# Kernel tuning notes

Hardware: AMD Instinct MI355X
Metric: run time of the kernel (lower is better)

The kernel has to match this reference:

```python
import math
import jax, jax.numpy as jnp
import numpy as np

D_MODEL = 512
H = 8          # head_num
HD = 64        # head_dim
ETA = 4
R = 8
D_FFC = 2048
EPS = 1e-6
GRU_BIAS = 2.0
T, B = 128, 32
TOTAL_PROJ = H * HD * 5 + H * ETA * 3  # 2656


def _layer_norm(x, g, b):
    m = x.mean(-1, keepdims=True)
    v = ((x - m) ** 2).mean(-1, keepdims=True)
    return (x - m) / jnp.sqrt(v + 1e-5) * g + b


def _outer(a, b):
    # a: (T,B,H,D), b: (T,B,H,E) -> (T,B,H,D*E), row-major over (D,E) like torch bmm+reshape
    t, bb, h, d = a.shape
    return (a[..., :, None] * b[..., None, :]).reshape(t, bb, h, d * b.shape[-1])


def _gru_gate(x, y, w, u):
    # GTrXL-style gating: x = residual stream, y = new signal. w,u: (3, d, d)
    r = jax.nn.sigmoid(y @ w[0].T + x @ u[0].T)
    z = jax.nn.sigmoid(y @ w[1].T + x @ u[1].T - GRU_BIAS)
    h = jnp.tanh(y @ w[2].T + (r * x) @ u[2].T)
    return (1.0 - z) * x + z * h


def _discounted_sum(prev, x, d):
    # y_t = d_t * y_{t-1} + x_t, y_{-1} = prev. x: (T, ...), d broadcastable to x.
    def step(c, xd):
        xi, di = xd
        nc = di * c + xi
        return nc, nc
    _, ys = jax.lax.scan(step, prev, (x, d))
    return ys


def setup_inputs() -> dict:
    key = jax.random.key(0)
    ks = jax.random.split(key, 12)
    sc_p = 1.0 / math.sqrt(D_MODEL)
    return {
        "inputs": jax.random.normal(ks[0], (T, B, D_MODEL), jnp.float32),
        "terminations": jax.random.randint(ks[1], (T, B), 0, 2).astype(jnp.int32),
        "tilde_k": jnp.zeros((B, R, H, ETA * HD), jnp.float32),
        "tilde_v": jnp.zeros((B, R, H, HD), jnp.float32),
        "s_prev": jnp.zeros((B, H, ETA * HD), jnp.float32),
        "tick": jnp.zeros((B, 1), jnp.float32),
        "w_proj": jax.random.normal(ks[2], (TOTAL_PROJ, D_MODEL), jnp.float32) * sc_p,
        "b_proj": jnp.zeros((TOTAL_PROJ,), jnp.float32),
        "w_attn": jax.random.normal(ks[3], (D_MODEL, H * HD), jnp.float32) * (1.0 / math.sqrt(H * HD)),
        "b_attn": jnp.zeros((D_MODEL,), jnp.float32),
        "ln1_g": jnp.ones((D_MODEL,), jnp.float32),
        "ln1_b": jnp.zeros((D_MODEL,), jnp.float32),
        "ln2_g": jnp.ones((D_MODEL,), jnp.float32),
        "ln2_b": jnp.zeros((D_MODEL,), jnp.float32),
        "gru1_w": jax.random.normal(ks[4], (3, D_MODEL, D_MODEL), jnp.float32) * sc_p,
        "gru1_u": jax.random.normal(ks[5], (3, D_MODEL, D_MODEL), jnp.float32) * sc_p,
        "gru2_w": jax.random.normal(ks[6], (3, D_MODEL, D_MODEL), jnp.float32) * sc_p,
        "gru2_u": jax.random.normal(ks[7], (3, D_MODEL, D_MODEL), jnp.float32) * sc_p,
        "ffc_w1": jax.random.normal(ks[8], (D_FFC, D_MODEL), jnp.float32) * sc_p,
        "ffc_b1": jnp.zeros((D_FFC,), jnp.float32),
        "ffc_w2": jax.random.normal(ks[9], (D_MODEL, D_FFC), jnp.float32) * (1.0 / math.sqrt(D_FFC)),
        "ffc_b2": jnp.zeros((D_MODEL,), jnp.float32),
    }


def _forward(inputs, terminations, tilde_k, tilde_v, s_prev, tick,
             w_proj, b_proj, w_attn, b_attn, ln1_g, ln1_b, ln2_g, ln2_b,
             gru1_w, gru1_u, gru2_w, gru2_u, ffc_w1, ffc_b1, ffc_w2, ffc_b2):
    t, bsz, _ = inputs.shape
    omegas = jnp.linspace(-math.pi, math.pi, R).astype(inputs.dtype)

    x_normed = _layer_norm(inputs, ln1_g, ln1_b)
    all_proj = x_normed @ w_proj.T + b_proj  # (T,B,2656)
    kqv_dim = H * HD * 5
    kqvbg = all_proj[..., :kqv_dim].reshape(t, bsz, H, 5, HD)
    p123 = all_proj[..., kqv_dim:].reshape(t, bsz, H, 3, ETA)

    keys = kqvbg[..., 0, :]
    queries = kqvbg[..., 1, :]
    values = kqvbg[..., 2, :]
    beta = jax.nn.sigmoid(kqvbg[..., 3, :])
    gammas = kqvbg[..., 4, :]
    p1, p2, p3 = p123[..., 0, :], p123[..., 1, :], p123[..., 2, :]

    keys_exp = _outer(jax.nn.relu(keys), jax.nn.relu(p1))          # (T,B,H,HD*ETA)
    queries_exp = _outer(jax.nn.relu(queries), jax.nn.relu(p2))
    gammas_exp = _outer(jax.nn.sigmoid(gammas), jax.nn.sigmoid(p3))

    ticks = tick[None] + jnp.arange(1, t + 1, dtype=tick.dtype).reshape(t, 1, 1)  # (T,B,1)
    occil = jnp.cos(ticks * omegas)  # (T,B,R)

    values_gated = values * beta                 # (T,B,H,HD)
    keys_gated = keys_exp * gammas_exp           # (T,B,H,HD*ETA)
    s_in = keys_gated
    values_osc = values_gated[:, :, None] * occil[..., None, None]  # (T,B,R,H,HD)
    keys_osc = keys_gated[:, :, None] * occil[..., None, None]      # (T,B,R,H,HD*ETA)

    term_mask = (1.0 - terminations.astype(inputs.dtype))[:, :, None, None]  # (T,B,1,1)
    discount_gamma = (1.0 - gammas_exp) * term_mask   # (T,B,H,HD*ETA)
    discount_beta = (1.0 - beta) * term_mask          # (T,B,H,HD)

    final_keys = _discounted_sum(tilde_k, keys_osc, discount_gamma[:, :, None])
    final_values = _discounted_sum(tilde_v, values_osc, discount_beta[:, :, None])
    final_s = _discounted_sum(s_prev, s_in, discount_gamma)

    kdq = (final_keys * queries_exp[:, :, None]).sum(-1)   # (T,B,R,H)
    kv = (final_values * kdq[..., None]).sum(2)             # (T,B,H,HD)
    norm = (final_s * queries_exp).sum(-1) + EPS            # (T,B,H)
    attn = kv / (2 * R * norm[..., None])
    attn = attn.reshape(t, bsz, H * HD) @ w_attn.T + b_attn  # (T,B,d_model)

    gating1 = _gru_gate(inputs, jax.nn.relu(attn), gru1_w, gru1_u)
    ffc_in = _layer_norm(gating1, ln2_g, ln2_b)
    ffc_out = jax.nn.relu(jax.nn.relu(ffc_in @ ffc_w1.T + ffc_b1) @ ffc_w2.T + ffc_b2)
    output = _gru_gate(gating1, ffc_out, gru2_w, gru2_u)
    return output


def reference(inputs, terminations, tilde_k, tilde_v, s_prev, tick,
              w_proj, b_proj, w_attn, b_attn, ln1_g, ln1_b, ln2_g, ln2_b,
              gru1_w, gru1_u, gru2_w, gru2_u, ffc_w1, ffc_b1, ffc_w2, ffc_b2):
    return _forward(inputs, terminations, tilde_k, tilde_v, s_prev, tick,
                    w_proj, b_proj, w_attn, b_attn, ln1_g, ln1_b, ln2_g, ln2_b,
                    gru1_w, gru1_u, gru2_w, gru2_u, ffc_w1, ffc_b1, ffc_w2, ffc_b2)
```

## Files before the change

kernel.cpp:

```cpp
#include <hip/hip_runtime.h>
#include <hip/hip_bf16.h>
#include <math.h>

#define DM   512
#define HH   8
#define RR   8
#define TT   128
#define BBATCH 32
#define MM   (TT*BBATCH)
#define NPROJ 2656
#define KQV  2560

typedef __attribute__((ext_vector_type(8))) short bf16x8;
typedef __attribute__((ext_vector_type(4))) float f32x4;

__device__ __forceinline__ float sigmoidf_(float x) {
    return 1.0f / (1.0f + __expf(-x));
}

__device__ __forceinline__ void gload_lds16(const void* g, void* l) {
    __builtin_amdgcn_global_load_lds(
        (const __attribute__((address_space(1))) unsigned int*)g,
        (__attribute__((address_space(3))) unsigned int*)l, 16, 0, 0);
}

template<int CTRL, int RMASK>
__device__ __forceinline__ float dpp_add_(float x) {
    union { float f; int i; } a, b;
    a.f = x;
    b.i = __builtin_amdgcn_update_dpp(0, a.i, CTRL, RMASK, 0xf, true);
    return x + b.f;
}
__device__ __forceinline__ float wave_sum_u(float x) {
    x = dpp_add_<0x111, 0xf>(x);
    x = dpp_add_<0x112, 0xf>(x);
    x = dpp_add_<0x114, 0xf>(x);
    x = dpp_add_<0x118, 0xf>(x);
    x = dpp_add_<0x142, 0xa>(x);
    x = dpp_add_<0x143, 0xc>(x);
    union { float f; int i; } s, t;
    s.f = x;
    t.i = __builtin_amdgcn_readlane(s.i, 63);
    return t.f;
}

struct F2B9 {
    const float* s[9];
    __hip_bfloat16* d[9];
    int cum[10];
};

__global__ __launch_bounds__(256) void f2b_ln_all(F2B9 a,
    const float* __restrict__ x, const float* __restrict__ g,
    const float* __restrict__ b, __hip_bfloat16* __restrict__ lnout)
{
    if (blockIdx.x < 8752) {
        int q = blockIdx.x * 256 + threadIdx.x;
        if (q >= a.cum[9]) return;
        int s = 0;
        #pragma unroll
        for (int i = 1; i < 9; ++i) s += (q >= a.cum[i]);
        int i4 = (q - a.cum[s]) * 4;
        float4 v = *(const float4*)(a.s[s] + i4);
        __hip_bfloat16* dst = a.d[s] + i4;
        dst[0] = __float2bfloat16(v.x);
        dst[1] = __float2bfloat16(v.y);
        dst[2] = __float2bfloat16(v.z);
        dst[3] = __float2bfloat16(v.w);
        return;
    }
    int row = blockIdx.x - 8752;
    int tid = threadIdx.x;
    const float* xr = x + (size_t)row * DM;
    float2 v = ((const float2*)xr)[tid];
    float s = v.x + v.y;
    #pragma unroll
    for (int off = 32; off; off >>= 1) s += __shfl_down(s, off);
    __shared__ float red[8];
    int wid = tid >> 6, lane = tid & 63;
    if (lane == 0) red[wid] = s;
    __syncthreads();
    if (tid == 0) red[0] = (red[0] + red[1] + red[2] + red[3]) * (1.0f / DM);
    __syncthreads();
    float mean = red[0];
    float dx = v.x - mean, dy = v.y - mean;
    float sq = dx*dx + dy*dy;
    #pragma unroll
    for (int off = 32; off; off >>= 1) sq += __shfl_down(sq, off);
    if (lane == 0) red[4 + wid] = sq;
    __syncthreads();
    if (tid == 0) red[1] = rsqrtf((red[4]+red[5]+red[6]+red[7]) * (1.0f/DM) + 1e-5f);
    __syncthreads();
    float rstd = red[1];
    float2 gg = ((const float2*)g)[tid];
    float2 bb = ((const float2*)b)[tid];
    __hip_bfloat16* orow = lnout + (size_t)row * DM;
    orow[2*tid+0] = __float2bfloat16(dx * rstd * gg.x + bb.x);
    orow[2*tid+1] = __float2bfloat16(dy * rstd * gg.y + bb.y);
}

__device__ __forceinline__ void gemm_core128(
    const __hip_bfloat16* __restrict__ A, const __hip_bfloat16* __restrict__ W,
    const float* __restrict__ bias,
    float* __restrict__ Cf, __hip_bfloat16* __restrict__ Cb,
    int N, int K, int act, int m0, int n0,
    __hip_bfloat16* As, __hip_bfloat16* Bs)
{
    int tid = threadIdx.x;
    int wave = tid >> 6, lane = tid & 63;
    int wm = (wave >> 1) * 64, wn = (wave & 1) * 64;
    int fr = lane & 15, fq = lane >> 4;

    f32x4 acc[4][4];
    #pragma unroll
    for (int i = 0; i < 4; ++i)
        #pragma unroll
        for (int j = 0; j < 4; ++j)
            acc[i][j] = (f32x4){0.f, 0.f, 0.f, 0.f};

    int sm0 = wave*16 + fr;
    int sm1 = sm0 + 64;
    int wr0 = n0 + sm0; if (wr0 >= N) wr0 = N - 1;
    int wr1 = n0 + sm1; if (wr1 >= N) wr1 = N - 1;
    const __hip_bfloat16* Ag0 = A + (size_t)(m0 + sm0) * K + fq*8;
    const __hip_bfloat16* Ag1 = A + (size_t)(m0 + sm1) * K + fq*8;
    const __hip_bfloat16* Wg0 = W + (size_t)wr0 * K + fq*8;
    const __hip_bfloat16* Wg1 = W + (size_t)wr1 * K + fq*8;

    for (int k0 = 0; k0 < K; k0 += 32) {
        gload_lds16(Ag0 + k0, As + (size_t)wave*512);
        gload_lds16(Ag1 + k0, As + (size_t)(wave+4)*512);
        gload_lds16(Wg0 + k0, Bs + (size_t)wave*512);
        gload_lds16(Wg1 + k0, Bs + (size_t)(wave+4)*512);
        __syncthreads();
        bf16x8 af[4], bfr[4];
        #pragma unroll
        for (int i = 0; i < 4; ++i) {
            af[i]  = *(const bf16x8*)(As + (size_t)(wm/16 + i)*512 + lane*8);
            bfr[i] = *(const bf16x8*)(Bs + (size_t)(wn/16 + i)*512 + lane*8);
        }
        #pragma unroll
        for (int mi = 0; mi < 4; ++mi)
            #pragma unroll
            for (int ni = 0; ni < 4; ++ni)
                acc[mi][ni] = __builtin_amdgcn_mfma_f32_16x16x32_bf16(
                    af[mi], bfr[ni], acc[mi][ni], 0, 0, 0);
        __syncthreads();
    }

    #pragma unroll
    for (int ni = 0; ni < 4; ++ni) {
        int n = n0 + wn + ni*16 + fr;
        bool nok = n < N;
        float bv = (bias && nok) ? bias[n] : 0.f;
        #pragma unroll
        for (int mi = 0; mi < 4; ++mi) {
            #pragma unroll
            for (int r = 0; r < 4; ++r) {
                int m = m0 + wm + mi*16 + fq*4 + r;
                float v = acc[mi][ni][r] + bv;
                if (act) v = fmaxf(v, 0.f);
                if (nok) {
                    size_t idx = (size_t)m * N + n;
                    if (Cf) Cf[idx] = v;
                    if (Cb) Cb[idx] = __float2bfloat16(v);
                }
            }
        }
    }
}

__global__ __launch_bounds__(256) void gemm_bf16(
    const __hip_bfloat16* __restrict__ A, const __hip_bfloat16* __restrict__ W,
    const float* __restrict__ bias,
    float* __restrict__ Cf, __hip_bfloat16* __restrict__ Cb,
    int N, int K, int act)
{
    __shared__ __attribute__((aligned(16))) __hip_bfloat16 As[8*512];
    __shared__ __attribute__((aligned(16))) __hip_bfloat16 Bs[8*512];
    gemm_core128(A, W, bias, Cf, Cb, N, K, act, blockIdx.y * 128, blockIdx.x * 128, As, Bs);
}

__global__ __launch_bounds__(256) void ffc1_bx_dual(
    const __hip_bfloat16* __restrict__ Aa, const __hip_bfloat16* __restrict__ Wa,
    const float* __restrict__ biasA, __hip_bfloat16* __restrict__ CbA,
    int Na, int splitX,
    const __hip_bfloat16* __restrict__ Ab, const __hip_bfloat16* __restrict__ Wb,
    float* __restrict__ CfB, int Nb, int K)
{
    __shared__ __attribute__((aligned(16))) __hip_bfloat16 As[8*512];
    __shared__ __attribute__((aligned(16))) __hip_bfloat16 Bs[8*512];
    int bx = blockIdx.x;
    if (bx < splitX)
        gemm_core128(Aa, Wa, biasA, nullptr, CbA, Na, K, 1, blockIdx.y*128, bx*128, As, Bs);
    else
        gemm_core128(Ab, Wb, nullptr, CfB, nullptr, Nb, K, 0, blockIdx.y*128, (bx-splitX)*128, As, Bs);
}

__global__ __launch_bounds__(256) void gemm_bf16_s(
    const __hip_bfloat16* __restrict__ A, const __hip_bfloat16* __restrict__ W,
    const float* __restrict__ bias,
    float* __restrict__ Cf, __hip_bfloat16* __restrict__ Cb,
    int N, int K, int act)
{
    __shared__ __attribute__((aligned(16))) __hip_bfloat16 As[4*512];
    __shared__ __attribute__((aligned(16))) __hip_bfloat16 Bs[4*512];
    int tid = threadIdx.x;
    int wave = tid >> 6, lane = tid & 63;
    int m0 = blockIdx.y * 64, n0 = blockIdx.x * 64;
    int wm = (wave >> 1) * 32, wn = (wave & 1) * 32;
    int fr = lane & 15, fq = lane >> 4;

    f32x4 acc[2][2];
    #pragma unroll
    for (int i = 0; i < 2; ++i)
        #pragma unroll
        for (int j = 0; j < 2; ++j)
            acc[i][j] = (f32x4){0.f, 0.f, 0.f, 0.f};

    const __hip_bfloat16* Ag = A + (size_t)(m0 + wave*16 + fr) * K + fq*8;
    int wr0 = n0 + wave*16 + fr; if (wr0 >= N) wr0 = N - 1;
    const __hip_bfloat16* Wg = W + (size_t)wr0 * K + fq*8;

    for (int k0 = 0; k0 < K; k0 += 32) {
        gload_lds16(Ag + k0, As + (size_t)wave*512);
        gload_lds16(Wg + k0, Bs + (size_t)wave*512);
        __syncthreads();
        bf16x8 af[2], bfr[2];
        #pragma unroll
        for (int i = 0; i < 2; ++i)
            af[i]  = *(const bf16x8*)(As + (size_t)(wm/16 + i)*512 + lane*8);
        #pragma unroll
        for (int j = 0; j < 2; ++j)
            bfr[j] = *(const bf16x8*)(Bs + (size_t)(wn/16 + j)*512 + lane*8);
        #pragma unroll
        for (int mi = 0; mi < 2; ++mi)
            #pragma unroll
            for (int ni = 0; ni < 2; ++ni)
                acc[mi][ni] = __builtin_amdgcn_mfma_f32_16x16x32_bf16(
                    af[mi], bfr[ni], acc[mi][ni], 0, 0, 0);
        __syncthreads();
    }

    #pragma unroll
    for (int ni = 0; ni < 2; ++ni) {
        int n = n0 + wn + ni*16 + fr;
        bool nok = n < N;
        float bv = (bias && nok) ? bias[n] : 0.f;
        #pragma unroll
        for (int mi = 0; mi < 2; ++mi) {
            #pragma unroll
            for (int r = 0; r < 4; ++r) {
                int m = m0 + wm + mi*16 + fq*4 + r;
                float v = acc[mi][ni][r] + bv;
                if (act) v = fmaxf(v, 0.f);
                if (nok) {
                    size_t idx = (size_t)m * N + n;
                    if (Cf) Cf[idx] = v;
                    if (Cb) Cb[idx] = __float2bfloat16(v);
                }
            }
        }
    }
}

__global__ __launch_bounds__(256) void gemm_gruA_64(
    const __hip_bfloat16* __restrict__ A, const __hip_bfloat16* __restrict__ W,
    const float* __restrict__ Bx, const float* __restrict__ x,
    __hip_bfloat16* __restrict__ rx, float* __restrict__ z,
    float* __restrict__ A1h)
{
    __shared__ __attribute__((aligned(16))) __hip_bfloat16 As[4*512];
    __shared__ __attribute__((aligned(16))) __hip_bfloat16 Bs[8*512];
    const int K = DM;
    int tid = threadIdx.x;
    int wave = tid >> 6, lane = tid & 63;
    int m0 = blockIdx.y * 64, n0 = blockIdx.x * 128;
    int wm = (wave >> 1) * 32, wn = (wave & 1) * 64;
    int fr = lane & 15, fq = lane >> 4;

    f32x4 acc[2][4];
    #pragma unroll
    for (int i = 0; i < 2; ++i)
        #pragma unroll
        for (int j = 0; j < 4; ++j)
            acc[i][j] = (f32x4){0.f, 0.f, 0.f, 0.f};

    const __hip_bfloat16* Ag  = A + (size_t)(m0 + wave*16 + fr) * K + fq*8;
    const __hip_bfloat16* Wg0 = W + (size_t)(n0 + wave*16 + fr) * K + fq*8;
    const __hip_bfloat16* Wg1 = Wg0 + (size_t)64 * K;

    for (int k0 = 0; k0 < K; k0 += 32) {
        gload_lds16(Ag  + k0, As + (size_t)wave*512);
        gload_lds16(Wg0 + k0, Bs + (size_t)wave*512);
        gload_lds16(Wg1 + k0, Bs + (size_t)(wave+4)*512);
        __syncthreads();
        bf16x8 af[2], bfr[4];
        #pragma unroll
        for (int i = 0; i < 2; ++i)
            af[i]  = *(const bf16x8*)(As + (size_t)(wm/16 + i)*512 + lane*8);
        #pragma unroll
        for (int j = 0; j < 4; ++j)
            bfr[j] = *(const bf16x8*)(Bs + (size_t)(wn/16 + j)*512 + lane*8);
        #pragma unroll
        for (int mi = 0; mi < 2; ++mi)
            #pragma unroll
            for (int ni = 0; ni < 4; ++ni)
                acc[mi][ni] = __builtin_amdgcn_mfma_f32_16x16x32_bf16(
                    af[mi], bfr[ni], acc[mi][ni], 0, 0, 0);
        __syncthreads();
    }

    #pragma unroll
    for (int ni = 0; ni < 4; ++ni) {
        int n = n0 + wn + ni*16 + fr;
        #pragma unroll
        for (int mi = 0; mi < 2; ++mi) {
            #pragma unroll
            for (int r = 0; r < 4; ++r) {
                int m = m0 + wm + mi*16 + fq*4 + r;
                float v = acc[mi][ni][r];
                size_t mb = (size_t)m;
                if (n0 < 512) {
                    float rpre = v + Bx[mb*1024 + n];
                    rx[mb*512 + n] =
                        __float2bfloat16(sigmoidf_(rpre) * x[mb*512 + n]);
                } else if (n0 < 1024) {
                    float zpre = v + Bx[mb*1024 + n] - 2.0f;
                    z[mb*512 + (n - 512)] = sigmoidf_(zpre);
                } else {
                    A1h[mb*512 + (n - 1024)] = v;
                }
            }
        }
    }
}

__global__ __launch_bounds__(256) void gemm_gruC2_s(
    const __hip_bfloat16* __restrict__ A, const __hip_bfloat16* __restrict__ W,
    const float* __restrict__ A1h, const float* __restrict__ z,
    const float* __restrict__ x, float* __restrict__ out)
{
    __shared__ __attribute__((aligned(16))) __hip_bfloat16 As[4*512];
    __shared__ __attribute__((aligned(16))) __hip_bfloat16 Bs[4*512];
    const int K = DM;
    int tid = threadIdx.x;
    int wave = tid >> 6, lane = tid & 63;
    int m0 = blockIdx.y * 64, n0 = blockIdx.x * 64;
    int wm = (wave >> 1) * 32, wn = (wave & 1) * 32;
    int fr = lane & 15, fq = lane >> 4;

    f32x4 acc[2][2];
    #pragma unroll
    for (int i = 0; i < 2; ++i)
        #pragma unroll
        for (int j = 0; j < 2; ++j)
            acc[i][j] = (f32x4){0.f, 0.f, 0.f, 0.f};

    const __hip_bfloat16* Ag = A + (size_t)(m0 + wave*16 + fr) * K + fq*8;
    const __hip_bfloat16* Wg = W + (size_t)(n0 + wave*16 + fr) * K + fq*8;

    for (int k0 = 0; k0 < K; k0 += 32) {
        gload_lds16(Ag + k0, As + (size_t)wave*512);
        gload_lds16(Wg + k0, Bs + (size_t)wave*512);
        __syncthreads();
        bf16x8 af[2], bfr[2];
        #pragma unroll
        for (int i = 0; i < 2; ++i)
            af[i]  = *(const bf16x8*)(As + (size_t)(wm/16 + i)*512 + lane*8);
        #pragma unroll
        for (int j = 0; j < 2; ++j)
            bfr[j] = *(const bf16x8*)(Bs + (size_t)(wn/16 + j)*512 + lane*8);
        #pragma unroll
        for (int mi = 0; mi < 2; ++mi)
            #pragma unroll
            for (int ni = 0; ni < 2; ++ni)
                acc[mi][ni] = __builtin_amdgcn_mfma_f32_16x16x32_bf16(
                    af[mi], bfr[ni], acc[mi][ni], 0, 0, 0);
        __syncthreads();
    }

    #pragma unroll
    for (int ni = 0; ni < 2; ++ni) {
        int n = n0 + wn + ni*16 + fr;
        #pragma unroll
        for (int mi = 0; mi < 2; ++mi) {
            #pragma unroll
            for (int r = 0; r < 4; ++r) {
                int m = m0 + wm + mi*16 + fq*4 + r;
                size_t i = (size_t)m * 512 + n;
                float hh = tanhf(A1h[i] + acc[mi][ni][r]);
                float zz = z[i];
                out[i] = (1.0f - zz) * x[i] + zz * hh;
            }
        }
    }
}

#define NCH   4
#define CHK   32
#define BNDF  (44*64)

__global__ __launch_bounds__(256) void scan_attn_fused(
    const float* __restrict__ proj, const int* __restrict__ term,
    const float* __restrict__ tick, const float* __restrict__ tilde_k,
    const float* __restrict__ tilde_v, const float* __restrict__ s_prev,
    __hip_bfloat16* __restrict__ attn,
    const __hip_bfloat16* __restrict__ gA, const __hip_bfloat16* __restrict__ gW,
    float* __restrict__ gC)
{
    extern __shared__ __attribute__((aligned(16))) char smem_dyn[];
    int bid = blockIdx.x;
    if (bid >= 256) {
        __hip_bfloat16* As = (__hip_bfloat16*)smem_dyn;
        __hip_bfloat16* Bs = As + 8*512;
        int g = bid - 256;
        gemm_core128(gA, gW, nullptr, gC, nullptr, 1024, DM, 0,
                     (g >> 3) * 128, (g & 7) * 128, As, Bs);
        return;
    }

    float* bnd  = (float*)smem_dyn;
    float* occt = bnd + 3*BNDF;
    int*   flags= (int*)(occt + TT*8);

    const int b = bid >> 3, h = bid & 7;
    const int tid = threadIdx.x;
    const int wv = tid >> 6, lane = tid & 63;
    const int t0 = wv * CHK;

    const float tk = tick[b];
    if (tid < 4) flags[tid] = 0;
    {
        const float PI_ = 3.14159265358979323846f;
        #pragma unroll
        for (int i = 0; i < 4; ++i) {
            int idx = tid*4 + i;
            int t = idx >> 3, r = idx & 7;
            float w = -PI_ + (float)r * (2.0f*PI_/7.0f);
            occt[idx] = cosf((tk + (float)(t + 1)) * w);
        }
    }
    __syncthreads();

    int tmv = (lane < CHK) ? term[(size_t)(t0 + lane)*BBATCH + b] : 0;

    float fs[4], fk[8][4], fv[8], Pg[4], Pb;

    auto zero_state = [&]() {
        #pragma unroll
        for (int j = 0; j < 4; ++j) fs[j] = 0.f;
        #pragma unroll
        for (int r = 0; r < 8; ++r) {
            #pragma unroll
            for (int j = 0; j < 4; ++j) fk[r][j] = 0.f;
            fv[r] = 0.f;
        }
    };
    auto load_init = [&]() {
        float4 s4 = *(const float4*)(s_prev + ((size_t)(b*HH + h))*256 + lane*4);
        fs[0]=s4.x; fs[1]=s4.y; fs[2]=s4.z; fs[3]=s4.w;
        #pragma unroll
        for (int r = 0; r < 8; ++r) {
            float4 k4 = *(const float4*)(tilde_k + (((size_t)b*RR + r)*HH + h)*256 + lane*4);
            fk[r][0]=k4.x; fk[r][1]=k4.y; fk[r][2]=k4.z; fk[r][3]=k4.w;
            fv[r] = tilde_v[(((size_t)b*RR + r)*HH + h)*64 + lane];
        }
    };
    auto load_bnd = [&](int w) {
        const float* p = bnd + w*BNDF;
        #pragma unroll
        for (int j = 0; j < 4; ++j) fs[j] = p[j*64 + lane];
        #pragma unroll
        for (int r = 0; r < 8; ++r) {
            #pragma unroll
            for (int j = 0; j < 4; ++j) fk[r][j] = p[(4 + r*4 + j)*64 + lane];
            fv[r] = p[(36 + r)*64 + lane];
        }
    };
    auto store_bnd = [&](int w) {
        float* p = bnd + w*BNDF;
        #pragma unroll
        for (int j = 0; j < 4; ++j) p[j*64 + lane] = fs[j];
        #pragma unroll
        for (int r = 0; r < 8; ++r) {
            #pragma unroll
            for (int j = 0; j < 4; ++j) p[(4 + r*4 + j)*64 + lane] = fk[r][j];
            p[(36 + r)*64 + lane] = fv[r];
        }
    };
    auto combine = [&](int w) {
        const float* p = bnd + w*BNDF;
        #pragma unroll
        for (int j = 0; j < 4; ++j) fs[j] = fmaf(Pg[j], p[j*64 + lane], fs[j]);
        #pragma unroll
        for (int r = 0; r < 8; ++r) {
            #pragma unroll
            for (int j = 0; j < 4; ++j)
                fk[r][j] = fmaf(Pg[j], p[(4 + r*4 + j)*64 + lane], fk[r][j]);
            fv[r] = fmaf(Pb, p[(36 + r)*64 + lane], fv[r]);
        }
    };

    struct Raw { float k, q, v, be, ga; float4 P1, P2, P3; };
    auto load_raw = [&](int t, Raw& rw) {
        const float* prow = proj + (size_t)(t*BBATCH + b) * NPROJ;
        const float* p5 = prow + h*320;
        rw.k  = p5[lane];
        rw.q  = p5[64  + lane];
        rw.v  = p5[128 + lane];
        rw.be = p5[192 + lane];
        rw.ga = p5[256 + lane];
        const float* pp = prow + KQV + h*12;
        rw.P1 = *(const float4*)(pp);
        rw.P2 = *(const float4*)(pp + 4);
        rw.P3 = *(const float4*)(pp + 8);
    };

    auto sweep = [&](bool out) {
        Pg[0]=Pg[1]=Pg[2]=Pg[3]=1.f; Pb=1.f;
        Raw cur, nxt;
        load_raw(t0, cur);
        for (int i = 0; i < CHK; ++i) {
            const int t = t0 + i;
            if (i + 1 < CHK) load_raw(t + 1, nxt);
            const int tm = __builtin_amdgcn_readlane(tmv, i);
            const float mask = 1.0f - (float)tm;
            float kr = fmaxf(cur.k, 0.f);
            float sg = sigmoidf_(cur.ga);
            float sb = sigmoidf_(cur.be);
            float vg = cur.v * sb;
            float db = (1.f - sb) * mask;
            float p1a[4] = {cur.P1.x, cur.P1.y, cur.P1.z, cur.P1.w};
            float p3a[4] = {cur.P3.x, cur.P3.y, cur.P3.z, cur.P3.w};
            float kg[4], dg[4];
            #pragma unroll
            for (int j = 0; j < 4; ++j) {
                float gexp = sg * sigmoidf_(p3a[j]);
                kg[j] = kr * fmaxf(p1a[j], 0.f) * gexp;
                dg[j] = (1.f - gexp) * mask;
            }
            float occ[8];
            {
                float4 o0 = *(const float4*)(occt + t*8);
                float4 o1 = *(const float4*)(occt + t*8 + 4);
                occ[0]=o0.x; occ[1]=o0.y; occ[2]=o0.z; occ[3]=o0.w;
                occ[4]=o1.x; occ[5]=o1.y; occ[6]=o1.z; occ[7]=o1.w;
            }
            #pragma unroll
            for (int j = 0; j < 4; ++j) {
                fs[j] = fmaf(dg[j], fs[j], kg[j]);
                Pg[j] *= dg[j];
            }
            #pragma unroll
            for (int r = 0; r < 8; ++r) {
                #pragma unroll
                for (int j = 0; j < 4; ++j)
                    fk[r][j] = fmaf(dg[j], fk[r][j], kg[j]*occ[r]);
                fv[r] = fmaf(db, fv[r], vg*occ[r]);
            }
            Pb *= db;
            if (out) {
                float qr = fmaxf(cur.q, 0.f);
                float p2a[4] = {cur.P2.x, cur.P2.y, cur.P2.z, cur.P2.w};
                float qe[4];
                #pragma unroll
                for (int j = 0; j < 4; ++j) qe[j] = qr * fmaxf(p2a[j], 0.f);
                float snorm = fs[0]*qe[0] + fs[1]*qe[1] + fs[2]*qe[2] + fs[3]*qe[3];
                float nrm_u = wave_sum_u(snorm);
                float kdq_u[8];
                #pragma unroll
                for (int r = 0; r < 8; ++r) {
                    float kdq = fk[r][0]*qe[0] + fk[r][1]*qe[1]
                              + fk[r][2]*qe[2] + fk[r][3]*qe[3];
                    kdq_u[r] = wave_sum_u(kdq);
                }
                float kv = 0.f;
                #pragma unroll
                for (int r = 0; r < 8; ++r) kv = fmaf(fv[r], kdq_u[r], kv);
                attn[(size_t)(t*BBATCH + b)*DM + h*64 + lane] =
                    __float2bfloat16(kv / (16.f * (nrm_u + 1e-6f)));
            }
            cur = nxt;
        }
    };

    if (wv < NCH - 1) {
        if (wv == 0) load_init(); else zero_state();
        sweep(false);
        if (wv > 0) {
            while (__hip_atomic_load(&flags[wv-1], __ATOMIC_ACQUIRE,
                                     __HIP_MEMORY_SCOPE_WORKGROUP) == 0)
                __builtin_amdgcn_s_sleep(1);
            combine(wv - 1);
        }
        store_bnd(wv);
        if (lane == 0)
            __hip_atomic_store(&flags[wv], 1, __ATOMIC_RELEASE,
                               __HIP_MEMORY_SCOPE_WORKGROUP);
    }

    if (wv == 0) {
        load_init();
    } else {
        while (__hip_atomic_load(&flags[wv-1], __ATOMIC_ACQUIRE,
                                 __HIP_MEMORY_SCOPE_WORKGROUP) == 0)
            __builtin_amdgcn_s_sleep(1);
        load_bnd(wv - 1);
    }
    sweep(true);
}

__global__ __launch_bounds__(256) void gru_final_ln(
    const float* __restrict__ A1h, const float* __restrict__ C2,
    const float* __restrict__ z, const float* __restrict__ x,
    const float* __restrict__ g, const float* __restrict__ bta,
    float* __restrict__ g1, __hip_bfloat16* __restrict__ g1b,
    __hip_bfloat16* __restrict__ fib)
{
    int row = blockIdx.x;
    int tid = threadIdx.x;
    size_t base = (size_t)row * DM;
    float2 c2v = ((const float2*)(C2 + base))[tid];
    float2 zv  = ((const float2*)(z  + base))[tid];
    float2 xv  = ((const float2*)(x  + base))[tid];
    float2 av  = ((const float2*)(A1h + base))[tid];
    float h0 = tanhf(av.x + c2v.x);
    float h1 = tanhf(av.y + c2v.y);
    float2 v;
    v.x = (1.0f - zv.x) * xv.x + zv.x * h0;
    v.y = (1.0f - zv.y) * xv.y + zv.y * h1;
    ((float2*)(g1 + base))[tid] = v;
    g1b[base + 2*tid+0] = __float2bfloat16(v.x);
    g1b[base + 2*tid+1] = __float2bfloat16(v.y);

    float s = v.x + v.y;
    #pragma unroll
    for (int off = 32; off; off >>= 1) s += __shfl_down(s, off);
    __shared__ float red[8];
    int wid = tid >> 6, lane = tid & 63;
    if (lane == 0) red[wid] = s;
    __syncthreads();
    if (tid == 0) red[0] = (red[0] + red[1] + red[2] + red[3]) * (1.0f / DM);
    __syncthreads();
    float mean = red[0];
    float dx = v.x - mean, dy = v.y - mean;
    float sq = dx*dx + dy*dy;
    #pragma unroll
    for (int off = 32; off; off >>= 1) sq += __shfl_down(sq, off);
    if (lane == 0) red[4 + wid] = sq;
    __syncthreads();
    if (tid == 0) red[1] = rsqrtf((red[4]+red[5]+red[6]+red[7]) * (1.0f/DM) + 1e-5f);
    __syncthreads();
    float rstd = red[1];
    float2 gg = ((const float2*)g)[tid];
    float2 bb = ((const float2*)bta)[tid];
    fib[base + 2*tid+0] = __float2bfloat16(dx * rstd * gg.x + bb.x);
    fib[base + 2*tid+1] = __float2bfloat16(dy * rstd * gg.y + bb.y);
}

extern "C" void kernel_launch(void* const* d_in, const int* in_sizes, int n_in,
                              void* d_out, int out_size, void* d_ws, size_t ws_size,
                              hipStream_t stream)
{
    const float* inputs = (const float*)d_in[0];
    const int*   term   = (const int*)  d_in[1];
    const float* tilde_k= (const float*)d_in[2];
    const float* tilde_v= (const float*)d_in[3];
    const float* s_prev = (const float*)d_in[4];
    const float* tick   = (const float*)d_in[5];
    const float* w_proj = (const float*)d_in[6];
    const float* b_proj = (const float*)d_in[7];
    const float* w_attn = (const float*)d_in[8];
    const float* b_attn = (const float*)d_in[9];
    const float* ln1_g  = (const float*)d_in[10];
    const float* ln1_b  = (const float*)d_in[11];
    const float* ln2_g  = (const float*)d_in[12];
    const float* ln2_b  = (const float*)d_in[13];
    const float* gru1_w = (const float*)d_in[14];
    const float* gru1_u = (const float*)d_in[15];
    const float* gru2_w = (const float*)d_in[16];
    const float* gru2_u = (const float*)d_in[17];
    const float* ffc_w1 = (const float*)d_in[18];
    const float* ffc_b1 = (const float*)d_in[19];
    const float* ffc_w2 = (const float*)d_in[20];
    const float* ffc_b2 = (const float*)d_in[21];
    float* out = (float*)d_out;
    float* ws  = (float*)d_ws;

    float* proj = ws;
    float* A1h  = ws;
    float* C2   = ws + 10878976;
    float* zb   = ws + 12976128;
    float* g1   = ws + 15073280;
    __hip_bfloat16* bb = (__hip_bfloat16*)(ws + 17170432);
    __hip_bfloat16* wp_bf  = bb + 0;
    __hip_bfloat16* wat_bf = bb + 1359872;
    __hip_bfloat16* g1w_bf = bb + 1622016;
    __hip_bfloat16* g1u_bf = bb + 2408448;
    __hip_bfloat16* g2w_bf = bb + 3194880;
    __hip_bfloat16* g2u_bf = bb + 3981312;
    __hip_bfloat16* fw1_bf = bb + 4767744;
    __hip_bfloat16* fw2_bf = bb + 5816320;
    __hip_bfloat16* in_bf  = bb + 6864896;
    __hip_bfloat16* xn_bf  = bb + 8962048;
    __hip_bfloat16* at_bf  = bb + 11059200;
    __hip_bfloat16* y1_bf  = bb + 13156352;
    __hip_bfloat16* rx_bf  = bb + 15253504;
    __hip_bfloat16* fi_bf  = bb + 17350656;
    __hip_bfloat16* mid_bf = bb + 19447808;
    __hip_bfloat16* fo_bf  = bb + 27836416;
    __hip_bfloat16* g1_bf  = bb + 29933568;
    float* Bx = ws + 33185792;

    dim3 blk(256);

    F2B9 fa;
    const float* srcs[9] = {w_proj, w_attn, gru1_w, gru1_u, gru2_w, gru2_u,
                            ffc_w1, ffc_w2, inputs};
    __hip_bfloat16* dsts[9] = {wp_bf, wat_bf, g1w_bf, g1u_bf, g2w_bf, g2u_bf,
                               fw1_bf, fw2_bf, in_bf};
    int quads[9] = {339968, 65536, 196608, 196608, 196608, 196608,
                    262144, 262144, 524288};
    int cum = 0;
    for (int i = 0; i < 9; ++i) { fa.s[i] = srcs[i]; fa.d[i] = dsts[i]; fa.cum[i] = cum; cum += quads[i]; }
    fa.cum[9] = cum;
    f2b_ln_all<<<8752 + MM, blk, 0, stream>>>(fa, inputs, ln1_g, ln1_b, xn_bf);

    gemm_bf16<<<dim3(21, 32), blk, 0, stream>>>(xn_bf, wp_bf, b_proj, proj, nullptr, NPROJ, DM, 0);

    size_t dyn = (size_t)(3*BNDF + TT*8 + 4) * 4;
    scan_attn_fused<<<512, blk, dyn, stream>>>(proj, term, tick, tilde_k, tilde_v,
                                               s_prev, at_bf, in_bf, g1u_bf, Bx);

    gemm_bf16_s<<<dim3(8, 64), blk, 0, stream>>>(at_bf, wat_bf, b_attn, nullptr, y1_bf, DM, DM, 1);

    gemm_gruA_64<<<dim3(12, 64), blk, 0, stream>>>(y1_bf, g1w_bf, Bx, inputs, rx_bf, zb, A1h);
    gemm_bf16_s<<<dim3(8, 64), blk, 0, stream>>>(rx_bf, g1u_bf + 2*DM*DM, nullptr, C2, nullptr, DM, DM, 0);
    gru_final_ln<<<MM, blk, 0, stream>>>(A1h, C2, zb, inputs, ln2_g, ln2_b, g1, g1_bf, fi_bf);

    ffc1_bx_dual<<<dim3(24, 32), blk, 0, stream>>>(fi_bf, fw1_bf, ffc_b1, mid_bf,
                                                   2048, 16,
                                                   g1_bf, g2u_bf, Bx, 1024, DM);

    gemm_bf16_s<<<dim3(8, 64), blk, 0, stream>>>(mid_bf, fw2_bf, ffc_b2, nullptr, fo_bf, DM, 2048, 1);

    gemm_gruA_64<<<dim3(12, 64), blk, 0, stream>>>(fo_bf, g2w_bf, Bx, g1, rx_bf, zb, A1h);
    gemm_gruC2_s<<<dim3(8, 64), blk, 0, stream>>>(rx_bf, g2u_bf + 2*DM*DM, A1h, zb, g1, out);
}
```

Baseline: 384.5 us.

## Overlap weight fp32-to-bf16 conversion with the projection GEMM launch

The first kernel now converts only w_proj and does the first layer norm. The remaining weight and input conversions move into extra blocks of the projection GEMM kernel, so they run alongside the GEMM tiles instead of on the critical path before it. This removes the serialization of the large conversion ahead of the GEMM. In exchange, the GEMM uses launch_bounds(256,1), which may change register allocation and occupancy.

After: 413.1 us. 7.4% more time.

```diff
diff --git a/kernel.cpp b/kernel.cpp
--- a/kernel.cpp
+++ b/kernel.cpp
@@ -44,32 +44,23 @@
     return t.f;
 }
 
-struct F2B9 {
-    const float* s[9];
-    __hip_bfloat16* d[9];
-    int cum[10];
-};
-
-__global__ __launch_bounds__(256) void f2b_ln_all(F2B9 a,
+__global__ __launch_bounds__(256) void f2b_wp_ln(
+    const float* __restrict__ wp, __hip_bfloat16* __restrict__ wpb,
     const float* __restrict__ x, const float* __restrict__ g,
     const float* __restrict__ b, __hip_bfloat16* __restrict__ lnout)
 {
-    if (blockIdx.x < 8752) {
+    if (blockIdx.x < 1328) {
         int q = blockIdx.x * 256 + threadIdx.x;
-        if (q >= a.cum[9]) return;
-        int s = 0;
-        #pragma unroll
-        for (int i = 1; i < 9; ++i) s += (q >= a.cum[i]);
-        int i4 = (q - a.cum[s]) * 4;
-        float4 v = *(const float4*)(a.s[s] + i4);
-        __hip_bfloat16* dst = a.d[s] + i4;
+        int i4 = q * 4;
+        float4 v = *(const float4*)(wp + i4);
+        __hip_bfloat16* dst = wpb + i4;
         dst[0] = __float2bfloat16(v.x);
         dst[1] = __float2bfloat16(v.y);
         dst[2] = __float2bfloat16(v.z);
         dst[3] = __float2bfloat16(v.w);
         return;
     }
-    int row = blockIdx.x - 8752;
+    int row = blockIdx.x - 1328;
     int tid = threadIdx.x;
     const float* xr = x + (size_t)row * DM;
     float2 v = ((const float2*)xr)[tid];
@@ -179,6 +170,38 @@
     __shared__ __attribute__((aligned(16))) __hip_bfloat16 As[8*512];
     __shared__ __attribute__((aligned(16))) __hip_bfloat16 Bs[8*512];
     gemm_core128(A, W, bias, Cf, Cb, N, K, act, blockIdx.y * 128, blockIdx.x * 128, As, Bs);
+}
+
+struct F2B8 {
+    const float* s[8];
+    __hip_bfloat16* d[8];
+    int cum[9];
+};
+
+__global__ __launch_bounds__(256, 1) void proj_conv(
+    const __hip_bfloat16* __restrict__ A, const __hip_bfloat16* __restrict__ W,
+    const float* __restrict__ bias, float* __restrict__ Cf, F2B8 a)
+{
+    __shared__ __attribute__((aligned(16))) __hip_bfloat16 As[8*512];
+    __shared__ __attribute__((aligned(16))) __hip_bfloat16 Bs[8*512];
+    if (blockIdx.x >= 21) {
+        int cid = (blockIdx.x - 21) * 32 + blockIdx.y;
+        int q = cid * 256 + threadIdx.x;
+        if (q >= a.cum[8]) return;
+        int s = 0;
+        #pragma unroll
+        for (int i = 1; i < 8; ++i) s += (q >= a.cum[i]);
+        int i4 = (q - a.cum[s]) * 4;
+        float4 v = *(const float4*)(a.s[s] + i4);
+        __hip_bfloat16* dst = a.d[s] + i4;
+        dst[0] = __float2bfloat16(v.x);
+        dst[1] = __float2bfloat16(v.y);
+        dst[2] = __float2bfloat16(v.z);
+        dst[3] = __float2bfloat16(v.w);
+        return;
+    }
+    gemm_core128(A, W, bias, Cf, nullptr, NPROJ, DM, 0,
+                 blockIdx.y * 128, blockIdx.x * 128, As, Bs);
 }
 
 __global__ __launch_bounds__(256) void ffc1_bx_dual(
@@ -715,19 +738,19 @@
 
     dim3 blk(256);
 
-    F2B9 fa;
-    const float* srcs[9] = {w_proj, w_attn, gru1_w, gru1_u, gru2_w, gru2_u,
+    f2b_wp_ln<<<1328 + MM, blk, 0, stream>>>(w_proj, wp_bf, inputs, ln1_g, ln1_b, xn_bf);
+
+    F2B8 fa;
+    const float* srcs[8] = {w_attn, gru1_w, gru1_u, gru2_w, gru2_u,
                             ffc_w1, ffc_w2, inputs};
-    __hip_bfloat16* dsts[9] = {wp_bf, wat_bf, g1w_bf, g1u_bf, g2w_bf, g2u_bf,
+    __hip_bfloat16* dsts[8] = {wat_bf, g1w_bf, g1u_bf, g2w_bf, g2u_bf,
                                fw1_bf, fw2_bf, in_bf};
-    int quads[9] = {339968, 65536, 196608, 196608, 196608, 196608,
+    int quads[8] = {65536, 196608, 196608, 196608, 196608,
                     262144, 262144, 524288};
     int cum = 0;
-    for (int i = 0; i < 9; ++i) { fa.s[i] = srcs[i]; fa.d[i] = dsts[i]; fa.cum[i] = cum; cum += quads[i]; }
-    fa.cum[9] = cum;
-    f2b_ln_all<<<8752 + MM, blk, 0, stream>>>(fa, inputs, ln1_g, ln1_b, xn_bf);
-
-    gemm_bf16<<<dim3(21, 32), blk, 0, stream>>>(xn_bf, wp_bf, b_proj, proj, nullptr, NPROJ, DM, 0);
+    for (int i = 0; i < 8; ++i) { fa.s[i] = srcs[i]; fa.d[i] = dsts[i]; fa.cum[i] = cum; cum += quads[i]; }
+    fa.cum[8] = cum;
+    proj_conv<<<dim3(21 + 232, 32), blk, 0, stream>>>(xn_bf, wp_bf, b_proj, proj, fa);
 
     size_t dyn = (size_t)(3*BNDF + TT*8 + 4) * 4;
     scan_attn_fused<<<512, blk, dyn, stream>>>(proj, term, tick, tilde_k, tilde_v,
```
